# Kernel tuning notes

Measured on AMD Instinct MI355X. Metric: run time of the kernel, lower is better.

Reference implementation:

```python
import jax, jax.numpy as jnp
import numpy as np

N, E, ET = 20000, 200000, 40000
D_IN, H, NEA, HL, OUT = 8, 128, 7, 128, 4
HC = H * NEA  # 896


def _init(k, shape, fan_in):
    return jax.random.normal(k, shape, jnp.float32) * (1.0 / np.sqrt(fan_in))


def setup_inputs() -> dict:
    key = jax.random.key(0)
    ks = list(jax.random.split(key, 16))
    return {
        "x": jax.random.normal(ks[0], (N, D_IN), jnp.float32),
        "edge_index": jax.random.randint(ks[1], (2, E), 0, N),
        "edge_attr": jax.random.uniform(ks[2], (E, NEA), jnp.float32),
        "edge_index_test": jax.random.randint(ks[3], (2, ET), 0, N),
        "W0": _init(ks[4], (NEA, D_IN, H), D_IN), "b0": jnp.zeros((NEA, H), jnp.float32),
        "W1": _init(ks[5], (HC, H), HC), "b1": jnp.zeros((H,), jnp.float32),
        "W2": _init(ks[6], (NEA, H, H), H), "b2": jnp.zeros((NEA, H), jnp.float32),
        "W3": _init(ks[7], (NEA, HC, H), HC), "b3": jnp.zeros((NEA, H), jnp.float32),
        "ew1": _init(ks[8], (NEA, NEA * 4), NEA), "eb1": jnp.zeros((NEA * 4,), jnp.float32),
        "ew2": _init(ks[9], (NEA * 4, NEA * 4), NEA * 4), "eb2": jnp.zeros((NEA * 4,), jnp.float32),
        "ew3": _init(ks[10], (NEA * 4, 1), NEA * 4), "eb3": jnp.zeros((1,), jnp.float32),
        "lw0": _init(ks[11], (2 * HC, HL), 2 * HC), "lb0": jnp.zeros((HL,), jnp.float32),
        "lwh": _init(ks[12], (3, HL, HL), HL), "lbh": jnp.zeros((3, HL), jnp.float32),
        "lw4": _init(ks[13], (HL, OUT), HL), "lb4": jnp.zeros((OUT,), jnp.float32),
    }


def _forward(x, edge_attr, W0, b0, W1, b1, W2, b2, W3, b3,
             ew1, eb1, ew2, eb2, ew3, eb3,
             lw0, lb0, lwh, lbh, lw4, lb4,
             edge_index, edge_index_test):
    n = x.shape[0]
    row, col = edge_index[0], edge_index[1]
    loop = jnp.arange(n)
    # PyG gcn_norm: append self-loops with weight 1
    rows = jnp.concatenate([row, loop])
    cols = jnp.concatenate([col, loop])

    def gcn_norm(w):
        w2 = jnp.concatenate([w, jnp.ones((n,), w.dtype)])
        deg = jax.ops.segment_sum(w2, cols, num_segments=n)
        dis = jnp.where(deg > 0, 1.0 / jnp.sqrt(deg), 0.0)
        return dis[rows] * w2 * dis[cols]  # [E+N]

    norms = [gcn_norm(edge_attr[:, i]) for i in range(NEA)]

    def conv(h, W, b, norm):
        m = (h @ W)[rows] * norm[:, None]  # [E+N, H] gathered messages
        return jax.ops.segment_sum(m, cols, num_segments=n) + b

    x1 = jax.nn.relu(jnp.concatenate([conv(x, W0[i], b0[i], norms[i]) for i in range(NEA)], -1))
    # multi_edge_to_one (edge_fc_layers[1]) -> scalar edge weight in (0,1)
    t = jax.nn.relu(edge_attr @ ew1 + eb1)
    t = jax.nn.relu(t @ ew2 + eb2)
    ew = jax.nn.sigmoid((t @ ew3 + eb3)[:, 0])
    x2 = jax.nn.relu(conv(x1, W1, b1, gcn_norm(ew)))
    x3 = jax.nn.relu(jnp.concatenate([conv(x2, W2[i], b2[i], norms[i]) for i in range(NEA)], -1))
    x4 = jax.nn.relu(jnp.concatenate([conv(x3, W3[i], b3[i], norms[i]) for i in range(NEA)], -1))
    # dropout(p=0.5) is identity in eval mode

    def link_mlp(e):
        h = jax.nn.relu(e @ lw0 + lb0)
        for i in range(3):
            h = jax.nn.relu(h @ lwh[i] + lbh[i])
        return h @ lw4 + lb4

    s, d = edge_index_test[0], edge_index_test[1]
    t1 = link_mlp(jnp.concatenate([x4[s], x4[d]], -1))
    t2 = link_mlp(jnp.concatenate([x4[d], x4[s]], -1))[:, jnp.array([0, 2, 1, 3])]
    return 0.5 * (t1 + t2)  # [E_test, 4]


def reference(x, edge_index, edge_attr, edge_index_test,
              W0, b0, W1, b1, W2, b2, W3, b3,
              ew1, eb1, ew2, eb2, ew3, eb3,
              lw0, lb0, lwh, lbh, lw4, lb4):
    return _forward(x, edge_attr, W0, b0, W1, b1, W2, b2, W3, b3,
                    ew1, eb1, ew2, eb2, ew3, eb3,
                    lw0, lb0, lwh, lbh, lw4, lb4,
                    edge_index, edge_index_test)
```

## Files before the change

### kernel.cpp

```cpp
#include <hip/hip_runtime.h>
#include <math.h>

#define NN 20000
#define NE 200000
#define NT 40000
#define HP 136

typedef _Float16 f16;
typedef __attribute__((ext_vector_type(8))) _Float16 f16x8;
typedef __attribute__((ext_vector_type(4))) float f32x4;
typedef __attribute__((ext_vector_type(2))) _Float16 h2;

__global__ void k_edge_mlp(const float* __restrict__ ea,
                           const float* __restrict__ w1, const float* __restrict__ b1,
                           const float* __restrict__ w2, const float* __restrict__ b2,
                           const float* __restrict__ w3, const float* __restrict__ b3,
                           const int* __restrict__ col,
                           float* __restrict__ out, int* __restrict__ cnt) {
  int e = blockIdx.x * 256 + threadIdx.x;
  if (e >= NE) return;
  atomicAdd(&cnt[col[e]], 1);
  float a[7];
#pragma unroll
  for (int i = 0; i < 7; i++) a[i] = ea[e * 7 + i];
  float t1[28];
#pragma unroll
  for (int j = 0; j < 28; j++) {
    float s = b1[j];
#pragma unroll
    for (int k = 0; k < 7; k++) s = fmaf(a[k], w1[k * 28 + j], s);
    t1[j] = fmaxf(s, 0.f);
  }
  float t2[28];
  for (int j = 0; j < 28; j++) {
    float s = b2[j];
    for (int k = 0; k < 28; k++) s = fmaf(t1[k], w2[k * 28 + j], s);
    t2[j] = fmaxf(s, 0.f);
  }
  float s = b3[0];
  for (int k = 0; k < 28; k++) s = fmaf(t2[k], w3[k], s);
  out[e] = 1.f / (1.f + expf(-s));
}

__global__ void k_scan(int* __restrict__ cnt, int* __restrict__ rowptr) {
  __shared__ int sums[256];
  __shared__ int offs[256];
  int t = threadIdx.x;
  const int CH = (NN + 255) / 256;
  int base = t * CH;
  int s = 0;
  for (int i = 0; i < CH; i++) { int idx = base + i; if (idx < NN) s += cnt[idx]; }
  sums[t] = s;
  __syncthreads();
  if (t == 0) {
    int acc = 0;
    for (int i = 0; i < 256; i++) { offs[i] = acc; acc += sums[i]; }
    rowptr[NN] = acc;
  }
  __syncthreads();
  int acc = offs[t];
  for (int i = 0; i < CH; i++) {
    int idx = base + i;
    if (idx < NN) {
      int cv = cnt[idx];
      rowptr[idx] = acc;
      cnt[idx] = acc;
      acc += cv;
    }
  }
}

__global__ void k_fill_csr(const int* __restrict__ col, int* __restrict__ cursor,
                           int* __restrict__ eid) {
  int e = blockIdx.x * 256 + threadIdx.x;
  if (e >= NE) return;
  int pos = atomicAdd(&cursor[col[e]], 1);
  eid[pos] = e;
}

__global__ __launch_bounds__(64) void k_deg_csr(const int* __restrict__ rowptr,
                                                const int* __restrict__ eid,
                                                const float* __restrict__ ea,
                                                const float* __restrict__ ewb,
                                                float* __restrict__ dis) {
  int t = threadIdx.x;
  int n = blockIdx.x * 8 + (t >> 3);
  int i = t & 7;
  if (n >= NN) return;
  float deg = 1.f;
  int s = rowptr[n], e2 = rowptr[n + 1];
  for (int p = s; p < e2; p++) {
    int e = eid[p];
    deg += (i < 7) ? ea[e * 7 + i] : ewb[e];
  }
  dis[i * NN + n] = rsqrtf(deg);
}

__global__ void k_csr_norms(const int* __restrict__ eid, const int* __restrict__ row,
                            const int* __restrict__ col, const float* __restrict__ ea,
                            const float* __restrict__ ew, const float* __restrict__ dis,
                            int* __restrict__ csr_src, float* __restrict__ csr_norm) {
  int p = blockIdx.x * 256 + threadIdx.x;
  if (p >= NE) return;
  int e = eid[p];
  int r = row[e], c = col[e];
  csr_src[p] = r;
#pragma unroll
  for (int i = 0; i < 7; i++)
    csr_norm[i * NE + p] = dis[i * NN + r] * ea[e * 7 + i] * dis[i * NN + c];
  csr_norm[7 * NE + p] = dis[7 * NN + r] * ew[e] * dis[7 * NN + c];
}

__global__ void k_wprep(const float* __restrict__ W, int ldW, size_t matOff, int K,
                        f16* __restrict__ WT) {
  int g = blockIdx.y;
  int idx = blockIdx.x * 256 + threadIdx.x;
  if (idx >= K * 128) return;
  int k = idx >> 7, n = idx & 127;
  float v = W[(size_t)g * matOff + (size_t)k * ldW + n];
  WT[(size_t)g * 128 * K + (size_t)n * K + k] = (f16)v;
}

template <int OUTM, bool RELU, bool BIAS, bool GROUP_A, bool SWIZZLE>
__global__ __launch_bounds__(256) void k_mgemm(
    const f16* __restrict__ A, const f16* __restrict__ BT,
    const float* __restrict__ bias,
    float* __restrict__ Cf, f16* __restrict__ Ch,
    int ldA, int M, int K, int NG, int GXp) {
  int rowT, g;
  if (SWIZZLE) {
    int b = blockIdx.x;
    int xcd = b & 7, s = b >> 3;
    g = s % NG;
    int lr = s / NG;
    rowT = lr * 8 + xcd;
    if (rowT >= GXp) return;
  } else {
    rowT = blockIdx.x;
    g = blockIdx.y;
  }
  __shared__ f16 smem[8192];
  const int tid = threadIdx.x;
  const int w = tid >> 6, lane = tid & 63;
  const int quad = lane >> 4, lc = lane & 15;
  const int wr = w >> 1, wc = w & 1;
  const int bm = rowT * 128;
  const int ldC = NG * 128;
  const int cb = g * 128;
  const int aoff = GROUP_A ? g * K : 0;
  const f16* Bg = BT + (size_t)g * 128 * K;
  const int srow = lane >> 2, skoff = (lane & 3) * 8;

  f32x4 acc[4][4] = {};

  for (int k0 = 0; k0 < K; k0 += 32) {
#pragma unroll
    for (int l = 0; l < 4; l++) {
      int c = w + l * 4;
      int t = c >> 3, r16 = c & 7;
      int rowi = r16 * 16 + srow;
      f16* ldst = smem + t * 4096 + r16 * 512;
      const f16* src;
      if (t == 0) {
        int gm = bm + rowi;
        if (gm > M - 1) gm = M - 1;
        src = A + (size_t)gm * ldA + aoff + k0 + skoff;
      } else {
        src = Bg + (size_t)rowi * K + k0 + skoff;
      }
      __builtin_amdgcn_global_load_lds(
          (const __attribute__((address_space(1))) void*)src,
          (__attribute__((address_space(3))) void*)ldst, 16, 0, 0);
    }
    __syncthreads();
    f16x8 bf[4];
#pragma unroll
    for (int nt = 0; nt < 4; nt++) {
      int r = wc * 64 + nt * 16 + lc;
      bf[nt] = *(const f16x8*)(smem + 4096 + r * 32 + quad * 8);
    }
#pragma unroll
    for (int mt = 0; mt < 4; mt++) {
      int r = wr * 64 + mt * 16 + lc;
      f16x8 ah = *(const f16x8*)(smem + r * 32 + quad * 8);
#pragma unroll
      for (int nt = 0; nt < 4; nt++) {
        acc[mt][nt] = __builtin_amdgcn_mfma_f32_16x16x32_f16(ah, bf[nt], acc[mt][nt], 0, 0, 0);
      }
    }
    __syncthreads();
  }

  float bv[4];
  if (BIAS) {
#pragma unroll
    for (int nt = 0; nt < 4; nt++) bv[nt] = bias[cb + wc * 64 + nt * 16 + lc];
  }
#pragma unroll
  for (int mt = 0; mt < 4; mt++) {
#pragma unroll
    for (int r = 0; r < 4; r++) {
      int gm = bm + wr * 64 + mt * 16 + quad * 4 + r;
      if (gm >= M) continue;
#pragma unroll
      for (int nt = 0; nt < 4; nt++) {
        float v = acc[mt][nt][r];
        if (BIAS) v += bv[nt];
        if (RELU) v = fmaxf(v, 0.f);
        size_t idx = (size_t)gm * ldC + cb + wc * 64 + nt * 16 + lc;
        if (OUTM == 1) Ch[idx] = (f16)v;
        else Cf[idx] = v;
      }
    }
  }
}

__global__ __launch_bounds__(448) void k_agg7(const f16* __restrict__ hW,
                                              const float* __restrict__ csr_norm,
                                              const float* __restrict__ dis,
                                              const int* __restrict__ rowptr,
                                              const int* __restrict__ csr_src,
                                              const float* __restrict__ bias,
                                              f16* __restrict__ outq) {
  int n = blockIdx.x;
  int f2 = threadIdx.x;
  int i = f2 >> 6;
  const h2* hw2 = (const h2*)hW;
  const float* nrm = csr_norm + (size_t)i * NE;
  float d = dis[i * NN + n];
  h2 sv = hw2[(size_t)n * 448 + f2];
  float ax = d * d * (float)sv.x, ay = d * d * (float)sv.y;
  int s = rowptr[n], e = rowptr[n + 1];
  int p = s;
  for (; p + 4 <= e; p += 4) {
    int s0 = csr_src[p], s1 = csr_src[p + 1], s2 = csr_src[p + 2], s3 = csr_src[p + 3];
    float n0 = nrm[p], n1 = nrm[p + 1], n2 = nrm[p + 2], n3 = nrm[p + 3];
    h2 v0 = hw2[(size_t)s0 * 448 + f2];
    h2 v1 = hw2[(size_t)s1 * 448 + f2];
    h2 v2 = hw2[(size_t)s2 * 448 + f2];
    h2 v3 = hw2[(size_t)s3 * 448 + f2];
    ax = fmaf(n0, (float)v0.x, ax); ay = fmaf(n0, (float)v0.y, ay);
    ax = fmaf(n1, (float)v1.x, ax); ay = fmaf(n1, (float)v1.y, ay);
    ax = fmaf(n2, (float)v2.x, ax); ay = fmaf(n2, (float)v2.y, ay);
    ax = fmaf(n3, (float)v3.x, ax); ay = fmaf(n3, (float)v3.y, ay);
  }
  for (; p < e; p++) {
    int s0 = csr_src[p];
    float n0 = nrm[p];
    h2 v0 = hw2[(size_t)s0 * 448 + f2];
    ax = fmaf(n0, (float)v0.x, ax); ay = fmaf(n0, (float)v0.y, ay);
  }
  h2 o;
  o.x = (f16)fmaxf(ax + bias[2 * f2], 0.f);
  o.y = (f16)fmaxf(ay + bias[2 * f2 + 1], 0.f);
  ((h2*)outq)[(size_t)n * 448 + f2] = o;
}

__global__ __launch_bounds__(256) void k_agg1(const f16* __restrict__ hW,
                                              const float* __restrict__ nrm,
                                              const float* __restrict__ dis_i,
                                              const int* __restrict__ rowptr,
                                              const int* __restrict__ csr_src,
                                              const float* __restrict__ bias,
                                              float* __restrict__ x2f) {
  int t = threadIdx.x;
  int n = blockIdx.x * 4 + (t >> 6);
  int f2 = t & 63;
  if (n >= NN) return;
  const h2* hw2 = (const h2*)hW;
  float d = dis_i[n];
  h2 sv = hw2[(size_t)n * 64 + f2];
  float ax = d * d * (float)sv.x, ay = d * d * (float)sv.y;
  int s = rowptr[n], e = rowptr[n + 1];
  int p = s;
  for (; p + 4 <= e; p += 4) {
    int s0 = csr_src[p], s1 = csr_src[p + 1], s2 = csr_src[p + 2], s3 = csr_src[p + 3];
    float n0 = nrm[p], n1 = nrm[p + 1], n2 = nrm[p + 2], n3 = nrm[p + 3];
    h2 v0 = hw2[(size_t)s0 * 64 + f2];
    h2 v1 = hw2[(size_t)s1 * 64 + f2];
    h2 v2 = hw2[(size_t)s2 * 64 + f2];
    h2 v3 = hw2[(size_t)s3 * 64 + f2];
    ax = fmaf(n0, (float)v0.x, ax); ay = fmaf(n0, (float)v0.y, ay);
    ax = fmaf(n1, (float)v1.x, ax); ay = fmaf(n1, (float)v1.y, ay);
    ax = fmaf(n2, (float)v2.x, ax); ay = fmaf(n2, (float)v2.y, ay);
    ax = fmaf(n3, (float)v3.x, ax); ay = fmaf(n3, (float)v3.y, ay);
  }
  for (; p < e; p++) {
    int s0 = csr_src[p];
    float n0 = nrm[p];
    h2 v0 = hw2[(size_t)s0 * 64 + f2];
    ax = fmaf(n0, (float)v0.x, ax); ay = fmaf(n0, (float)v0.y, ay);
  }
  x2f[(size_t)n * 128 + 2 * f2] = fmaxf(ax + bias[2 * f2], 0.f);
  x2f[(size_t)n * 128 + 2 * f2 + 1] = fmaxf(ay + bias[2 * f2 + 1], 0.f);
}

__global__ __launch_bounds__(256) void k_agg2(const float* __restrict__ x2f,
                                              const float* __restrict__ csr_norm,
                                              const float* __restrict__ dis,
                                              const int* __restrict__ rowptr,
                                              const int* __restrict__ csr_src,
                                              f16* __restrict__ oq) {
  int t = threadIdx.x;
  int n = blockIdx.x * 4 + (t >> 6);
  int f2 = t & 63;
  if (n >= NN) return;
  const float2* x2 = (const float2*)x2f;
  float2 sv = x2[(size_t)n * 64 + f2];
  float ax[7], ay[7];
#pragma unroll
  for (int i = 0; i < 7; i++) {
    float d = dis[i * NN + n];
    ax[i] = d * d * sv.x;
    ay[i] = d * d * sv.y;
  }
  int s = rowptr[n], e = rowptr[n + 1];
  int p = s;
  for (; p + 2 <= e; p += 2) {
    int s0 = csr_src[p], s1 = csr_src[p + 1];
    float2 v0 = x2[(size_t)s0 * 64 + f2];
    float2 v1 = x2[(size_t)s1 * 64 + f2];
#pragma unroll
    for (int i = 0; i < 7; i++) {
      float n0 = csr_norm[(size_t)i * NE + p];
      float n1 = csr_norm[(size_t)i * NE + p + 1];
      ax[i] = fmaf(n0, v0.x, ax[i]); ay[i] = fmaf(n0, v0.y, ay[i]);
      ax[i] = fmaf(n1, v1.x, ax[i]); ay[i] = fmaf(n1, v1.y, ay[i]);
    }
  }
  for (; p < e; p++) {
    int s0 = csr_src[p];
    float2 v0 = x2[(size_t)s0 * 64 + f2];
#pragma unroll
    for (int i = 0; i < 7; i++) {
      float n0 = csr_norm[(size_t)i * NE + p];
      ax[i] = fmaf(n0, v0.x, ax[i]); ay[i] = fmaf(n0, v0.y, ay[i]);
    }
  }
#pragma unroll
  for (int i = 0; i < 7; i++) {
    h2 o;
    o.x = (f16)ax[i];
    o.y = (f16)ay[i];
    ((h2*)oq)[(size_t)n * 448 + i * 64 + f2] = o;
  }
}

__global__ __launch_bounds__(64) void k_agg_x(const float* __restrict__ x,
                                              const float* __restrict__ csr_norm,
                                              const float* __restrict__ dis,
                                              const int* __restrict__ rowptr,
                                              const int* __restrict__ csr_src,
                                              float* __restrict__ xagg) {
  int n = blockIdx.x;
  int f = threadIdx.x;
  if (f >= 56) return;
  int i = f >> 3, c = f & 7;
  float d = dis[i * NN + n];
  float acc = d * d * x[(size_t)n * 8 + c];
  int s = rowptr[n], e = rowptr[n + 1];
  for (int p = s; p < e; p++)
    acc = fmaf(csr_norm[i * NE + p], x[(size_t)csr_src[p] * 8 + c], acc);
  xagg[(size_t)n * 56 + f] = acc;
}

__global__ __launch_bounds__(896) void k_gemm0(const float* __restrict__ xagg,
                                               const float* __restrict__ W0,
                                               const float* __restrict__ b0,
                                               f16* __restrict__ outq) {
  int n = blockIdx.x;
  int f = threadIdx.x;
  int i = f >> 7, h = f & 127;
  float s = b0[i * 128 + h];
#pragma unroll
  for (int c = 0; c < 8; c++)
    s = fmaf(xagg[(size_t)n * 56 + i * 8 + c], W0[(i * 8 + c) * 128 + h], s);
  outq[(size_t)n * 896 + f] = (f16)fmaxf(s, 0.f);
}

__global__ __launch_bounds__(256) void k_link_fused(
    const float* __restrict__ UV, const int* __restrict__ eit,
    const float* __restrict__ lb0, const f16* __restrict__ lwht,
    const float* __restrict__ lbh, const float* __restrict__ lw4,
    const float* __restrict__ lb4, float* __restrict__ out) {
  __shared__ f16 Hhi[64 * HP];
  __shared__ f16 Hlo[64 * HP];
  __shared__ f16 Wt[128 * HP];
  __shared__ float ob[64][4];
  const int tid = threadIdx.x;
  const int t0 = blockIdx.x * 32;
  {
    int c = tid & 127;
    int rbase = tid >> 7;
    for (int it = 0; it < 32; it++) {
      int rr = rbase + it * 2;
      int tp = t0 + (rr >> 1), dir = rr & 1;
      int s = eit[tp], d = eit[NT + tp];
      int a = dir ? d : s, b = dir ? s : d;
      float v = UV[(size_t)a * 256 + c] + UV[(size_t)b * 256 + 128 + c] + lb0[c];
      v = fmaxf(v, 0.f);
      f16 h = (f16)v;
      Hhi[rr * HP + c] = h;
      Hlo[rr * HP + c] = (f16)(v - (float)h);
    }
  }
  const int w = tid >> 6, lane = tid & 63;
  const int quad = lane >> 4, lc = lane & 15;
  for (int l = 0; l < 3; l++) {
    __syncthreads();
    {
      const f16* src = lwht + (size_t)l * 128 * 128;
#pragma unroll
      for (int it = 0; it < 8; it++) {
        int idx = (tid + it * 256) * 8;
        int n = idx >> 7, k = idx & 127;
        *(float4*)&Wt[n * HP + k] = *(const float4*)&src[idx];
      }
    }
    __syncthreads();
    f32x4 acc[8] = {};
    const int arow = w * 16 + lc;
#pragma unroll
    for (int k0 = 0; k0 < 128; k0 += 32) {
      f16x8 ah = *(const f16x8*)&Hhi[arow * HP + k0 + quad * 8];
      f16x8 al = *(const f16x8*)&Hlo[arow * HP + k0 + quad * 8];
#pragma unroll
      for (int nt = 0; nt < 8; nt++) {
        f16x8 bf = *(const f16x8*)&Wt[(nt * 16 + lc) * HP + k0 + quad * 8];
        acc[nt] = __builtin_amdgcn_mfma_f32_16x16x32_f16(ah, bf, acc[nt], 0, 0, 0);
        acc[nt] = __builtin_amdgcn_mfma_f32_16x16x32_f16(al, bf, acc[nt], 0, 0, 0);
      }
    }
#pragma unroll
    for (int nt = 0; nt < 8; nt++) {
      int col = nt * 16 + lc;
      float bb = lbh[l * 128 + col];
#pragma unroll
      for (int r = 0; r < 4; r++) {
        int rrow = w * 16 + quad * 4 + r;
        float v = fmaxf(acc[nt][r] + bb, 0.f);
        f16 h = (f16)v;
        Hhi[rrow * HP + col] = h;
        Hlo[rrow * HP + col] = (f16)(v - (float)h);
      }
    }
  }
  __syncthreads();
  {
    int rr = tid >> 2, j = tid & 3;
    float o = lb4[j];
    for (int k = 0; k < 128; k++) {
      float hv = (float)Hhi[rr * HP + k] + (float)Hlo[rr * HP + k];
      o = fmaf(hv, lw4[k * 4 + j], o);
    }
    ob[rr][j] = o;
  }
  __syncthreads();
  if (tid < 128) {
    int tp = tid >> 2, j = tid & 3;
    const int perm[4] = {0, 2, 1, 3};
    out[(size_t)(t0 + tp) * 4 + j] = 0.5f * (ob[2 * tp][j] + ob[2 * tp + 1][perm[j]]);
  }
}

extern "C" void kernel_launch(void* const* d_in, const int* in_sizes, int n_in,
                              void* d_out, int out_size, void* d_ws, size_t ws_size,
                              hipStream_t stream) {
  const float* x   = (const float*)d_in[0];
  const int*   ei  = (const int*)d_in[1];
  const float* ea  = (const float*)d_in[2];
  const int*   eit = (const int*)d_in[3];
  const float* W0  = (const float*)d_in[4];
  const float* b0  = (const float*)d_in[5];
  const float* W1  = (const float*)d_in[6];
  const float* b1  = (const float*)d_in[7];
  const float* W2  = (const float*)d_in[8];
  const float* b2  = (const float*)d_in[9];
  const float* W3  = (const float*)d_in[10];
  const float* b3  = (const float*)d_in[11];
  const float* ew1 = (const float*)d_in[12];
  const float* eb1 = (const float*)d_in[13];
  const float* ew2 = (const float*)d_in[14];
  const float* eb2 = (const float*)d_in[15];
  const float* ew3 = (const float*)d_in[16];
  const float* eb3 = (const float*)d_in[17];
  const float* lw0 = (const float*)d_in[18];
  const float* lb0 = (const float*)d_in[19];
  const float* lwh = (const float*)d_in[20];
  const float* lbh = (const float*)d_in[21];
  const float* lw4 = (const float*)d_in[22];
  const float* lb4 = (const float*)d_in[23];
  const int* row = ei;
  const int* col = ei + NE;
  float* out = (float*)d_out;

  char* ws = (char*)d_ws;
  size_t off = 0;
  auto alloc = [&](size_t bytes) -> char* {
    char* p = ws + off;
    off += (bytes + 255) & ~(size_t)255;
    return p;
  };
  f16*   xA     = (f16*)alloc((size_t)NN * 896 * 2);
  f16*   xB     = (f16*)alloc((size_t)NN * 896 * 2);
  float* x2f    = (float*)alloc((size_t)NN * 128 * 4);
  float* UV     = (float*)alloc((size_t)NN * 256 * 4);
  float* csr_nrm= (float*)alloc((size_t)8 * NE * 4);
  float* dis    = (float*)alloc((size_t)8 * NN * 4);
  float* ewb    = (float*)alloc((size_t)NE * 4);
  int*   rowptr = (int*)alloc((size_t)(NN + 1) * 4);
  int*   cursor = (int*)alloc((size_t)NN * 4);
  int*   eid    = (int*)alloc((size_t)NE * 4);
  int*   csr_src= (int*)alloc((size_t)NE * 4);
  f16* w1t  = (f16*)alloc((size_t)128 * 896 * 2);
  f16* w2t  = (f16*)alloc((size_t)7 * 128 * 128 * 2);
  f16* w3t  = (f16*)alloc((size_t)7 * 128 * 896 * 2);
  f16* lw0t = (f16*)alloc((size_t)2 * 128 * 896 * 2);
  f16* lwht = (f16*)alloc((size_t)3 * 128 * 128 * 2);
  float* xagg = UV;
  (void)ws_size; (void)in_sizes; (void)n_in; (void)out_size;

  const int EB = (NE + 255) / 256;
  const int GX = (NN + 127) / 128;
  const int MC = (GX + 7) / 8;

  k_wprep<<<dim3(448, 1), 256, 0, stream>>>(W1, 128, 0, 896, w1t);
  k_wprep<<<dim3(64, 7), 256, 0, stream>>>(W2, 128, (size_t)128 * 128, 128, w2t);
  k_wprep<<<dim3(448, 7), 256, 0, stream>>>(W3, 128, (size_t)896 * 128, 896, w3t);
  k_wprep<<<dim3(448, 2), 256, 0, stream>>>(lw0, 128, (size_t)896 * 128, 896, lw0t);
  k_wprep<<<dim3(64, 3), 256, 0, stream>>>(lwh, 128, (size_t)128 * 128, 128, lwht);

  hipMemsetAsync(cursor, 0, (size_t)NN * 4, stream);
  k_edge_mlp<<<EB, 256, 0, stream>>>(ea, ew1, eb1, ew2, eb2, ew3, eb3, col, ewb, cursor);
  k_scan<<<1, 256, 0, stream>>>(cursor, rowptr);
  k_fill_csr<<<EB, 256, 0, stream>>>(col, cursor, eid);
  k_deg_csr<<<(NN + 7) / 8, 64, 0, stream>>>(rowptr, eid, ea, ewb, dis);
  k_csr_norms<<<EB, 256, 0, stream>>>(eid, row, col, ea, ewb, dis, csr_src, csr_nrm);

  k_agg_x<<<NN, 64, 0, stream>>>(x, csr_nrm, dis, rowptr, csr_src, xagg);
  k_gemm0<<<NN, 896, 0, stream>>>(xagg, W0, b0, xA);

  k_mgemm<1, false, false, false, false><<<dim3(GX, 1), 256, 0, stream>>>(
      xA, w1t, nullptr, nullptr, xB, 896, NN, 896, 1, GX);
  k_agg1<<<(NN + 3) / 4, 256, 0, stream>>>(xB, csr_nrm + (size_t)7 * NE,
                                           dis + (size_t)7 * NN, rowptr, csr_src, b1, x2f);

  k_agg2<<<(NN + 3) / 4, 256, 0, stream>>>(x2f, csr_nrm, dis, rowptr, csr_src, xB);
  k_mgemm<1, true, true, true, false><<<dim3(GX, 7), 256, 0, stream>>>(
      xB, w2t, b2, nullptr, xA, 896, NN, 128, 7, GX);

  k_mgemm<1, false, false, false, true><<<dim3(8 * MC * 7), 256, 0, stream>>>(
      xA, w3t, nullptr, nullptr, xB, 896, NN, 896, 7, GX);
  k_agg7<<<NN, 448, 0, stream>>>(xB, csr_nrm, dis, rowptr, csr_src, b3, xA);

  k_mgemm<0, false, false, false, true><<<dim3(8 * MC * 2), 256, 0, stream>>>(
      xA, lw0t, nullptr, UV, nullptr, 896, NN, 896, 2, GX);

  k_link_fused<<<NT / 32, 256, 0, stream>>>(UV, eit, lb0, lwht, lbh, lw4, lb4, out);
}
```

Measured before the change: 598.6 us.

## Fuse weight prep and layer0 kernels, deepen gather unrolling, store x2 in fp16

The five weight-transpose launches and the cursor memset become one kernel. The layer-0 aggregation and its small GEMM become one block-per-node kernel, with the edge loop split across 7 thread groups and reduced in shared memory. The gather loops in agg7, agg1 and agg2 are unrolled further to keep more loads in flight. The intermediate x2 is stored as fp16 instead of fp32, halving the gather traffic in agg2 at some cost in precision. The main aim is fewer launches and less memory traffic.

```diff
diff --git a/kernel.cpp b/kernel.cpp
--- a/kernel.cpp
+++ b/kernel.cpp
@@ -111,14 +111,40 @@
   csr_norm[7 * NE + p] = dis[7 * NN + r] * ew[e] * dis[7 * NN + c];
 }
 
-__global__ void k_wprep(const float* __restrict__ W, int ldW, size_t matOff, int K,
-                        f16* __restrict__ WT) {
-  int g = blockIdx.y;
-  int idx = blockIdx.x * 256 + threadIdx.x;
-  if (idx >= K * 128) return;
+__global__ void k_wprep_all(const float* __restrict__ W1, const float* __restrict__ W2,
+                            const float* __restrict__ W3, const float* __restrict__ lw0,
+                            const float* __restrict__ lwh,
+                            f16* __restrict__ w1t, f16* __restrict__ w2t,
+                            f16* __restrict__ w3t, f16* __restrict__ lw0t,
+                            f16* __restrict__ lwht, int* __restrict__ cursor) {
+  int b = blockIdx.x, t = threadIdx.x;
+  const float* W;
+  f16* D;
+  int K, g, tile;
+  size_t matOff;
+  if (b < 448) {
+    W = W1; D = w1t; K = 896; g = 0; tile = b; matOff = 0;
+  } else if (b < 896) {
+    int l = b - 448; W = W2; D = w2t; K = 128; g = l >> 6; tile = l & 63;
+    matOff = 16384;
+  } else if (b < 4032) {
+    int l = b - 896; W = W3; D = w3t; K = 896; g = l / 448; tile = l % 448;
+    matOff = 114688;
+  } else if (b < 4928) {
+    int l = b - 4032; W = lw0; D = lw0t; K = 896; g = l / 448; tile = l % 448;
+    matOff = 114688;
+  } else if (b < 5120) {
+    int l = b - 4928; W = lwh; D = lwht; K = 128; g = l >> 6; tile = l & 63;
+    matOff = 16384;
+  } else {
+    int idx = (b - 5120) * 256 + t;
+    if (idx < NN) cursor[idx] = 0;
+    return;
+  }
+  int idx = tile * 256 + t;
   int k = idx >> 7, n = idx & 127;
-  float v = W[(size_t)g * matOff + (size_t)k * ldW + n];
-  WT[(size_t)g * 128 * K + (size_t)n * K + k] = (f16)v;
+  float v = W[(size_t)g * matOff + (size_t)k * 128 + n];
+  D[(size_t)g * 128 * K + (size_t)n * K + k] = (f16)v;
 }
 
 template <int OUTM, bool RELU, bool BIAS, bool GROUP_A, bool SWIZZLE>
@@ -232,6 +258,20 @@
   float ax = d * d * (float)sv.x, ay = d * d * (float)sv.y;
   int s = rowptr[n], e = rowptr[n + 1];
   int p = s;
+  for (; p + 8 <= e; p += 8) {
+    int si[8];
+    float nn_[8];
+    h2 vv[8];
+#pragma unroll
+    for (int u = 0; u < 8; u++) { si[u] = csr_src[p + u]; nn_[u] = nrm[p + u]; }
+#pragma unroll
+    for (int u = 0; u < 8; u++) vv[u] = hw2[(size_t)si[u] * 448 + f2];
+#pragma unroll
+    for (int u = 0; u < 8; u++) {
+      ax = fmaf(nn_[u], (float)vv[u].x, ax);
+      ay = fmaf(nn_[u], (float)vv[u].y, ay);
+    }
+  }
   for (; p + 4 <= e; p += 4) {
     int s0 = csr_src[p], s1 = csr_src[p + 1], s2 = csr_src[p + 2], s3 = csr_src[p + 3];
     float n0 = nrm[p], n1 = nrm[p + 1], n2 = nrm[p + 2], n3 = nrm[p + 3];
@@ -262,7 +302,7 @@
                                               const int* __restrict__ rowptr,
                                               const int* __restrict__ csr_src,
                                               const float* __restrict__ bias,
-                                              float* __restrict__ x2f) {
+                                              f16* __restrict__ x2h) {
   int t = threadIdx.x;
   int n = blockIdx.x * 4 + (t >> 6);
   int f2 = t & 63;
@@ -273,17 +313,19 @@
   float ax = d * d * (float)sv.x, ay = d * d * (float)sv.y;
   int s = rowptr[n], e = rowptr[n + 1];
   int p = s;
-  for (; p + 4 <= e; p += 4) {
-    int s0 = csr_src[p], s1 = csr_src[p + 1], s2 = csr_src[p + 2], s3 = csr_src[p + 3];
-    float n0 = nrm[p], n1 = nrm[p + 1], n2 = nrm[p + 2], n3 = nrm[p + 3];
-    h2 v0 = hw2[(size_t)s0 * 64 + f2];
-    h2 v1 = hw2[(size_t)s1 * 64 + f2];
-    h2 v2 = hw2[(size_t)s2 * 64 + f2];
-    h2 v3 = hw2[(size_t)s3 * 64 + f2];
-    ax = fmaf(n0, (float)v0.x, ax); ay = fmaf(n0, (float)v0.y, ay);
-    ax = fmaf(n1, (float)v1.x, ax); ay = fmaf(n1, (float)v1.y, ay);
-    ax = fmaf(n2, (float)v2.x, ax); ay = fmaf(n2, (float)v2.y, ay);
-    ax = fmaf(n3, (float)v3.x, ax); ay = fmaf(n3, (float)v3.y, ay);
+  for (; p + 8 <= e; p += 8) {
+    int si[8];
+    float nn_[8];
+    h2 vv[8];
+#pragma unroll
+    for (int u = 0; u < 8; u++) { si[u] = csr_src[p + u]; nn_[u] = nrm[p + u]; }
+#pragma unroll
+    for (int u = 0; u < 8; u++) vv[u] = hw2[(size_t)si[u] * 64 + f2];
+#pragma unroll
+    for (int u = 0; u < 8; u++) {
+      ax = fmaf(nn_[u], (float)vv[u].x, ax);
+      ay = fmaf(nn_[u], (float)vv[u].y, ay);
+    }
   }
   for (; p < e; p++) {
     int s0 = csr_src[p];
@@ -291,11 +333,13 @@
     h2 v0 = hw2[(size_t)s0 * 64 + f2];
     ax = fmaf(n0, (float)v0.x, ax); ay = fmaf(n0, (float)v0.y, ay);
   }
-  x2f[(size_t)n * 128 + 2 * f2] = fmaxf(ax + bias[2 * f2], 0.f);
-  x2f[(size_t)n * 128 + 2 * f2 + 1] = fmaxf(ay + bias[2 * f2 + 1], 0.f);
-}
-
-__global__ __launch_bounds__(256) void k_agg2(const float* __restrict__ x2f,
+  h2 o;
+  o.x = (f16)fmaxf(ax + bias[2 * f2], 0.f);
+  o.y = (f16)fmaxf(ay + bias[2 * f2 + 1], 0.f);
+  ((h2*)x2h)[(size_t)n * 64 + f2] = o;
+}
+
+__global__ __launch_bounds__(256) void k_agg2(const f16* __restrict__ x2h,
                                               const float* __restrict__ csr_norm,
                                               const float* __restrict__ dis,
                                               const int* __restrict__ rowptr,
@@ -305,36 +349,43 @@
   int n = blockIdx.x * 4 + (t >> 6);
   int f2 = t & 63;
   if (n >= NN) return;
-  const float2* x2 = (const float2*)x2f;
-  float2 sv = x2[(size_t)n * 64 + f2];
+  const h2* x2 = (const h2*)x2h;
+  h2 svh = x2[(size_t)n * 64 + f2];
+  float svx = (float)svh.x, svy = (float)svh.y;
   float ax[7], ay[7];
 #pragma unroll
   for (int i = 0; i < 7; i++) {
     float d = dis[i * NN + n];
-    ax[i] = d * d * sv.x;
-    ay[i] = d * d * sv.y;
+    ax[i] = d * d * svx;
+    ay[i] = d * d * svy;
   }
   int s = rowptr[n], e = rowptr[n + 1];
   int p = s;
-  for (; p + 2 <= e; p += 2) {
-    int s0 = csr_src[p], s1 = csr_src[p + 1];
-    float2 v0 = x2[(size_t)s0 * 64 + f2];
-    float2 v1 = x2[(size_t)s1 * 64 + f2];
+  for (; p + 4 <= e; p += 4) {
+    int si[4];
+    h2 vv[4];
+#pragma unroll
+    for (int u = 0; u < 4; u++) si[u] = csr_src[p + u];
+#pragma unroll
+    for (int u = 0; u < 4; u++) vv[u] = x2[(size_t)si[u] * 64 + f2];
 #pragma unroll
     for (int i = 0; i < 7; i++) {
-      float n0 = csr_norm[(size_t)i * NE + p];
-      float n1 = csr_norm[(size_t)i * NE + p + 1];
-      ax[i] = fmaf(n0, v0.x, ax[i]); ay[i] = fmaf(n0, v0.y, ay[i]);
-      ax[i] = fmaf(n1, v1.x, ax[i]); ay[i] = fmaf(n1, v1.y, ay[i]);
+#pragma unroll
+      for (int u = 0; u < 4; u++) {
+        float nw = csr_norm[(size_t)i * NE + p + u];
+        ax[i] = fmaf(nw, (float)vv[u].x, ax[i]);
+        ay[i] = fmaf(nw, (float)vv[u].y, ay[i]);
+      }
     }
   }
   for (; p < e; p++) {
     int s0 = csr_src[p];
-    float2 v0 = x2[(size_t)s0 * 64 + f2];
+    h2 v0 = x2[(size_t)s0 * 64 + f2];
 #pragma unroll
     for (int i = 0; i < 7; i++) {
-      float n0 = csr_norm[(size_t)i * NE + p];
-      ax[i] = fmaf(n0, v0.x, ax[i]); ay[i] = fmaf(n0, v0.y, ay[i]);
+      float nw = csr_norm[(size_t)i * NE + p];
+      ax[i] = fmaf(nw, (float)v0.x, ax[i]);
+      ay[i] = fmaf(nw, (float)v0.y, ay[i]);
     }
   }
 #pragma unroll
@@ -346,36 +397,46 @@
   }
 }
 
-__global__ __launch_bounds__(64) void k_agg_x(const float* __restrict__ x,
-                                              const float* __restrict__ csr_norm,
-                                              const float* __restrict__ dis,
-                                              const int* __restrict__ rowptr,
-                                              const int* __restrict__ csr_src,
-                                              float* __restrict__ xagg) {
+__global__ __launch_bounds__(896) void k_layer0(const float* __restrict__ x,
+                                                const float* __restrict__ csr_norm,
+                                                const float* __restrict__ dis,
+                                                const int* __restrict__ rowptr,
+                                                const int* __restrict__ csr_src,
+                                                const float* __restrict__ W0,
+                                                const float* __restrict__ b0,
+                                                f16* __restrict__ outq) {
+  __shared__ float part[7][56];
+  __shared__ float xaggs[56];
   int n = blockIdx.x;
-  int f = threadIdx.x;
-  if (f >= 56) return;
-  int i = f >> 3, c = f & 7;
-  float d = dis[i * NN + n];
-  float acc = d * d * x[(size_t)n * 8 + c];
+  int t = threadIdx.x;
   int s = rowptr[n], e = rowptr[n + 1];
-  for (int p = s; p < e; p++)
-    acc = fmaf(csr_norm[i * NE + p], x[(size_t)csr_src[p] * 8 + c], acc);
-  xagg[(size_t)n * 56 + f] = acc;
-}
-
-__global__ __launch_bounds__(896) void k_gemm0(const float* __restrict__ xagg,
-                                               const float* __restrict__ W0,
-                                               const float* __restrict__ b0,
-                                               f16* __restrict__ outq) {
-  int n = blockIdx.x;
-  int f = threadIdx.x;
-  int i = f >> 7, h = f & 127;
-  float s = b0[i * 128 + h];
+  if (t < 448) {
+    int grp = t >> 6;
+    int idx = t & 63;
+    if (idx < 56) {
+      int i = idx >> 3, c = idx & 7;
+      float acc = 0.f;
+      for (int p = s + grp; p < e; p += 7)
+        acc = fmaf(csr_norm[i * NE + p], x[(size_t)csr_src[p] * 8 + c], acc);
+      part[grp][idx] = acc;
+    }
+  }
+  __syncthreads();
+  if (t < 56) {
+    int i = t >> 3, c = t & 7;
+    float d = dis[i * NN + n];
+    float acc = d * d * x[(size_t)n * 8 + c];
+#pragma unroll
+    for (int grp = 0; grp < 7; grp++) acc += part[grp][t];
+    xaggs[t] = acc;
+  }
+  __syncthreads();
+  int i = t >> 7, h = t & 127;
+  float sum = b0[i * 128 + h];
 #pragma unroll
   for (int c = 0; c < 8; c++)
-    s = fmaf(xagg[(size_t)n * 56 + i * 8 + c], W0[(i * 8 + c) * 128 + h], s);
-  outq[(size_t)n * 896 + f] = (f16)fmaxf(s, 0.f);
+    sum = fmaf(xaggs[i * 8 + c], W0[(i * 8 + c) * 128 + h], sum);
+  outq[(size_t)n * 896 + t] = (f16)fmaxf(sum, 0.f);
 }
 
 __global__ __launch_bounds__(256) void k_link_fused(
@@ -503,7 +564,7 @@
   };
   f16*   xA     = (f16*)alloc((size_t)NN * 896 * 2);
   f16*   xB     = (f16*)alloc((size_t)NN * 896 * 2);
-  float* x2f    = (float*)alloc((size_t)NN * 128 * 4);
+  f16*   x2h    = (f16*)alloc((size_t)NN * 128 * 2);
   float* UV     = (float*)alloc((size_t)NN * 256 * 4);
   float* csr_nrm= (float*)alloc((size_t)8 * NE * 4);
   float* dis    = (float*)alloc((size_t)8 * NN * 4);
@@ -517,35 +578,29 @@
   f16* w3t  = (f16*)alloc((size_t)7 * 128 * 896 * 2);
   f16* lw0t = (f16*)alloc((size_t)2 * 128 * 896 * 2);
   f16* lwht = (f16*)alloc((size_t)3 * 128 * 128 * 2);
-  float* xagg = UV;
   (void)ws_size; (void)in_sizes; (void)n_in; (void)out_size;
 
   const int EB = (NE + 255) / 256;
   const int GX = (NN + 127) / 128;
   const int MC = (GX + 7) / 8;
 
-  k_wprep<<<dim3(448, 1), 256, 0, stream>>>(W1, 128, 0, 896, w1t);
-  k_wprep<<<dim3(64, 7), 256, 0, stream>>>(W2, 128, (size_t)128 * 128, 128, w2t);
-  k_wprep<<<dim3(448, 7), 256, 0, stream>>>(W3, 128, (size_t)896 * 128, 896, w3t);
-  k_wprep<<<dim3(448, 2), 256, 0, stream>>>(lw0, 128, (size_t)896 * 128, 896, lw0t);
-  k_wprep<<<dim3(64, 3), 256, 0, stream>>>(lwh, 128, (size_t)128 * 128, 128, lwht);
-
-  hipMemsetAsync(cursor, 0, (size_t)NN * 4, stream);
+  k_wprep_all<<<5120 + (NN + 255) / 256, 256, 0, stream>>>(
+      W1, W2, W3, lw0, lwh, w1t, w2t, w3t, lw0t, lwht, cursor);
+
   k_edge_mlp<<<EB, 256, 0, stream>>>(ea, ew1, eb1, ew2, eb2, ew3, eb3, col, ewb, cursor);
   k_scan<<<1, 256, 0, stream>>>(cursor, rowptr);
   k_fill_csr<<<EB, 256, 0, stream>>>(col, cursor, eid);
   k_deg_csr<<<(NN + 7) / 8, 64, 0, stream>>>(rowptr, eid, ea, ewb, dis);
   k_csr_norms<<<EB, 256, 0, stream>>>(eid, row, col, ea, ewb, dis, csr_src, csr_nrm);
 
-  k_agg_x<<<NN, 64, 0, stream>>>(x, csr_nrm, dis, rowptr, csr_src, xagg);
-  k_gemm0<<<NN, 896, 0, stream>>>(xagg, W0, b0, xA);
+  k_layer0<<<NN, 896, 0, stream>>>(x, csr_nrm, dis, rowptr, csr_src, W0, b0, xA);
 
   k_mgemm<1, false, false, false, false><<<dim3(GX, 1), 256, 0, stream>>>(
       xA, w1t, nullptr, nullptr, xB, 896, NN, 896, 1, GX);
   k_agg1<<<(NN + 3) / 4, 256, 0, stream>>>(xB, csr_nrm + (size_t)7 * NE,
-                                           dis + (size_t)7 * NN, rowptr, csr_src, b1, x2f);
-
-  k_agg2<<<(NN + 3) / 4, 256, 0, stream>>>(x2f, csr_nrm, dis, rowptr, csr_src, xB);
+                                           dis + (size_t)7 * NN, rowptr, csr_src, b1, x2h);
+
+  k_agg2<<<(NN + 3) / 4, 256, 0, stream>>>(x2h, csr_nrm, dis, rowptr, csr_src, xB);
   k_mgemm<1, true, true, true, false><<<dim3(GX, 7), 256, 0, stream>>>(
       xB, w2t, b2, nullptr, xA, 896, NN, 128, 7, GX);
 
```

Result: no change. 599.7 us (+0.2%).
